# Optimization experiments

Hardware: AMD Instinct MI355X
Metric: run time of the kernel (lower is better)

## Reference

```python
import jax, jax.numpy as jnp
import numpy as np

V = 54  # len(nonterminals)
D = 512  # term_embedding_dim
LEAVES = 60000
LEVELS = 10


def _structure():
    rng = np.random.default_rng(0)
    sizes = [LEAVES]
    for _ in range(LEVELS - 1):
        sizes.append(sizes[-1] // 2)
    starts = np.concatenate([[0], np.cumsum(sizes)]).astype(np.int64)
    N = int(starts[-1])
    node_types = rng.integers(0, V, N).astype(np.int32)
    edge_child, edge_parent, edge_starts = [], [], [0, 0]
    for l in range(1, LEVELS):
        n_l = sizes[l]
        c1 = rng.integers(starts[l - 1], starts[l], n_l)  # child at height l-1 (defines height)
        c2 = rng.integers(0, starts[l], n_l)              # second child anywhere below
        edge_child.append(np.stack([c1, c2], 1).ravel())
        edge_parent.append(np.repeat(np.arange(n_l), 2))
        edge_starts.append(edge_starts[-1] + 2 * n_l)
    edge_child = np.concatenate(edge_child).astype(np.int64)
    edge_parent = np.concatenate(edge_parent).astype(np.int64)
    edge_starts = np.asarray(edge_starts, dtype=np.int64)
    roots = np.arange(starts[-2], starts[-1], dtype=np.int64)  # top-level nodes
    return node_types, starts, edge_child, edge_parent, edge_starts, roots


def setup_inputs() -> dict:
    node_types, level_starts, edge_child, edge_parent_local, edge_level_starts, roots = _structure()
    key = jax.random.key(0)
    ks = jax.random.split(key, 9)
    k = 1.0 / np.sqrt(D)
    u = lambda kk, shape: jax.random.uniform(kk, shape, jnp.float32, -k, k)
    return {
        "node_types": jnp.asarray(node_types),
        "level_starts": level_starts,
        "edge_child": jnp.asarray(edge_child),
        "edge_parent_local": jnp.asarray(edge_parent_local),
        "edge_level_starts": edge_level_starts,
        "roots": jnp.asarray(roots),
        "W_if": u(ks[0], (D, V)),
        "W_hf": u(ks[1], (D, D)),
        "b_f": u(ks[2], (D,)),
        "W_i": u(ks[3], (D, V + D)),
        "b_i": u(ks[4], (D,)),
        "W_o": u(ks[5], (D, V + D)),
        "b_o": u(ks[6], (D,)),
        "W_u": u(ks[7], (D, V + D)),
        "b_u": u(ks[8], (D,)),
    }


def reference(node_types, level_starts, edge_child, edge_parent_local, edge_level_starts,
              roots, W_if, W_hf, b_f, W_i, b_i, W_o, b_o, W_u, b_u):
    ls = np.asarray(level_starts)
    es = np.asarray(edge_level_starts)
    N = int(ls[-1])
    dt = W_if.dtype
    H = jnp.zeros((N, D), dtype=dt)
    C = jnp.zeros((N, D), dtype=dt)
    for l in range(len(ls) - 1):
        s, e = int(ls[l]), int(ls[l + 1])
        n = e - s
        x = jax.nn.one_hot(node_types[s:e], V, dtype=dt)  # [n, V]
        if l == 0:
            h_sum = jnp.zeros((n, D), dtype=dt)
            c_remain = jnp.zeros((n, D), dtype=dt)
        else:
            a, b = int(es[l]), int(es[l + 1])
            ci = edge_child[a:b]
            pj = edge_parent_local[a:b]
            h_ch = H[ci]  # [e_l, D] gather of children hidden states
            c_ch = C[ci]
            h_sum = jax.ops.segment_sum(h_ch, pj, num_segments=n)
            Wx = x @ W_if.T  # [n, D]
            f = jax.nn.sigmoid(Wx[pj] + h_ch @ W_hf.T + b_f)  # per-edge forget gates
            c_remain = jax.ops.segment_sum(f * c_ch, pj, num_segments=n)
        xh = jnp.concatenate([x, h_sum], axis=1)  # [n, V+D]
        i_g = jax.nn.sigmoid(xh @ W_i.T + b_i)
        o_g = jax.nn.sigmoid(xh @ W_o.T + b_o)
        u = jnp.tanh(xh @ W_u.T + b_u)
        cells = i_g * u + c_remain
        hid = o_g * jnp.tanh(cells)
        H = H.at[s:e].set(hid)
        C = C.at[s:e].set(cells)
    return H[roots]
```

## Files before the change

kernel.cpp:

```cpp
#include <hip/hip_runtime.h>
#include <hip/hip_bf16.h>

#define DD 512
#define VV 54
#define NLEAF 60000
#define NINT 59881

typedef __attribute__((ext_vector_type(8))) short bf16x8;
typedef __attribute__((ext_vector_type(4))) float f32x4;

__device__ __forceinline__ float bflo(unsigned int u) {
    union { unsigned int i; float f; } v; v.i = u << 16; return v.f;
}
__device__ __forceinline__ float bfhi(unsigned int u) {
    union { unsigned int i; float f; } v; v.i = u & 0xffff0000u; return v.f;
}
__device__ __forceinline__ float bfu2f(unsigned short u) {
    union { unsigned int i; float f; } v; v.i = ((unsigned int)u) << 16; return v.f;
}
__device__ __forceinline__ unsigned short f2bfu(float f) {
    union { unsigned int i; float f; } v; v.f = f;
    unsigned int x = v.i;
    return (unsigned short)((x + 0x7FFFu + ((x >> 16) & 1u)) >> 16);
}
__device__ __forceinline__ unsigned int pack2(float lo, float hi) {
    return (unsigned int)f2bfu(lo) | ((unsigned int)f2bfu(hi) << 16);
}
__device__ __forceinline__ float b2f(__hip_bfloat16 x) { return __bfloat162float(x); }
__device__ __forceinline__ float sigm(float x) { return 1.f / (1.f + __expf(-x)); }

__device__ __forceinline__ void ld8(const __hip_bfloat16* p, float* o) {
    uint4 v = *(const uint4*)p;
    const unsigned short* s = (const unsigned short*)&v;
#pragma unroll
    for (int j = 0; j < 8; j++) o[j] = bfu2f(s[j]);
}
__device__ __forceinline__ void ldf8(const float* p, float* o) {
    float4 a = *(const float4*)p, b = *(const float4*)(p + 4);
    o[0] = a.x; o[1] = a.y; o[2] = a.z; o[3] = a.w;
    o[4] = b.x; o[5] = b.y; o[6] = b.z; o[7] = b.w;
}

__global__ void detect_idx64(const int* __restrict__ ec, int* __restrict__ flag) {
    __shared__ int nz;
    if (threadIdx.x == 0) nz = 0;
    __syncthreads();
    if (ec[2 * threadIdx.x + 1] != 0) atomicAdd(&nz, 1);
    __syncthreads();
    if (threadIdx.x == 0) flag[0] = (nz == 0) ? 1 : 0;
}

__global__ void prep_tables(const float* __restrict__ W_if, const float* __restrict__ b_f,
                            const float* __restrict__ W_i, const float* __restrict__ b_i,
                            const float* __restrict__ W_o, const float* __restrict__ b_o,
                            const float* __restrict__ W_u, const float* __restrict__ b_u,
                            float* __restrict__ wifc, float* __restrict__ tbi,
                            float* __restrict__ tbo, float* __restrict__ tbu,
                            __hip_bfloat16* __restrict__ hleaf, __hip_bfloat16* __restrict__ cleaf) {
    int t = blockIdx.x;
    for (int d = threadIdx.x; d < DD; d += blockDim.x) {
        wifc[t * DD + d] = W_if[d * VV + t] + b_f[d];
        float vi = W_i[d * (VV + DD) + t] + b_i[d];
        float vo = W_o[d * (VV + DD) + t] + b_o[d];
        float vu = W_u[d * (VV + DD) + t] + b_u[d];
        tbi[t * DD + d] = vi; tbo[t * DD + d] = vo; tbu[t * DD + d] = vu;
        float gi = sigm(vi), go = sigm(vo), gu = tanhf(vu);
        float c = gi * gu;
        float h = go * tanhf(c);
        hleaf[t * DD + d] = __float2bfloat16(h);
        cleaf[t * DD + d] = __float2bfloat16(c);
    }
}

__global__ void prep_wall(const float* __restrict__ W_hf, const float* __restrict__ W_i,
                          const float* __restrict__ W_o, const float* __restrict__ W_u,
                          __hip_bfloat16* __restrict__ Wall) {
    int idx = blockIdx.x * 256 + threadIdx.x;
    int m = idx >> 18;
    int rem = idx & (DD * DD - 1);
    float v;
    if (m == 0) {
        v = W_hf[rem];
    } else {
        int d = rem >> 9, k = rem & 511;
        const float* W = (m == 1) ? W_i : ((m == 2) ? W_o : W_u);
        v = W[d * (VV + DD) + VV + k];
    }
    Wall[idx] = __float2bfloat16(v);
}

__global__ void prep_pleaf(const __hip_bfloat16* __restrict__ hleaf,
                           const __hip_bfloat16* __restrict__ Wall,
                           __hip_bfloat16* __restrict__ Pleaf) {
    __shared__ float hsh[DD];
    int tt = blockIdx.x;
    int cb = blockIdx.y;
    for (int k = threadIdx.x; k < DD; k += 256) hsh[k] = b2f(hleaf[tt * DD + k]);
    __syncthreads();
    int c = cb * 256 + threadIdx.x;
    const __hip_bfloat16* wrow = Wall + (size_t)c * DD;
    float s = 0.f;
#pragma unroll 4
    for (int kq = 0; kq < 64; kq++) {
        uint4 v = *(const uint4*)(wrow + kq * 8);
        const unsigned short* vs = (const unsigned short*)&v;
#pragma unroll
        for (int e = 0; e < 8; e++) s += bfu2f(vs[e]) * hsh[kq * 8 + e];
    }
    Pleaf[(size_t)tt * 2048 + c] = __float2bfloat16(s);
}

__device__ __forceinline__ const __hip_bfloat16* h_row(int ci,
        const __hip_bfloat16* __restrict__ Hint, const __hip_bfloat16* __restrict__ hleaf,
        const int* __restrict__ nt) {
    return (ci < NLEAF) ? (hleaf + (size_t)nt[ci] * DD) : (Hint + (size_t)(ci - NLEAF) * DD);
}
__device__ __forceinline__ const __hip_bfloat16* c_row(int ci,
        const __hip_bfloat16* __restrict__ Cint, const __hip_bfloat16* __restrict__ cleaf,
        const int* __restrict__ nt) {
    return (ci < NLEAF) ? (cleaf + (size_t)nt[ci] * DD) : (Cint + (size_t)(ci - NLEAF) * DD);
}

__global__ __launch_bounds__(256) void gather_cell(
    const __hip_bfloat16* __restrict__ Pleaf,
    const __hip_bfloat16* __restrict__ cleaf,
    const int* __restrict__ nt, const int* __restrict__ ecb, int eoff,
    const int* __restrict__ ntl, const float* __restrict__ wifc,
    const float* __restrict__ tbi, const float* __restrict__ tbo,
    const float* __restrict__ tbu,
    __hip_bfloat16* __restrict__ Hout, __hip_bfloat16* __restrict__ Cout,
    const int* __restrict__ idx64, int n) {
    int idx = blockIdx.x * 256 + threadIdx.x;
    int p = idx >> 6;
    if (p >= n) return;
    const int mode = idx64[0];
    const int d0 = (idx & 63) << 3;
    int c1 = ecb[(eoff + 2 * p) << mode];
    int c2 = ecb[(eoff + 2 * p + 1) << mode];
    int t1 = nt[c1], t2 = nt[c2];
    int tp = ntl[p];
    const __hip_bfloat16* P1 = Pleaf + (size_t)t1 * 2048;
    const __hip_bfloat16* P2 = Pleaf + (size_t)t2 * 2048;
    float f1[8], f2v[8], i1[8], i2[8], o1[8], o2[8], u1[8], u2[8], x1[8], x2[8];
    ld8(P1 + d0, f1);         ld8(P2 + d0, f2v);
    ld8(P1 + 512 + d0, i1);   ld8(P2 + 512 + d0, i2);
    ld8(P1 + 1024 + d0, o1);  ld8(P2 + 1024 + d0, o2);
    ld8(P1 + 1536 + d0, u1);  ld8(P2 + 1536 + d0, u2);
    ld8(cleaf + (size_t)t1 * DD + d0, x1);
    ld8(cleaf + (size_t)t2 * DD + d0, x2);
    float wf[8], vb[8], ob[8], ub[8];
    ldf8(wifc + (size_t)tp * DD + d0, wf);
    ldf8(tbi + (size_t)tp * DD + d0, vb);
    ldf8(tbo + (size_t)tp * DD + d0, ob);
    ldf8(tbu + (size_t)tp * DD + d0, ub);
    float hv[8], cv[8];
#pragma unroll
    for (int j = 0; j < 8; j++) {
        float fr = sigm(f1[j] + wf[j]) * x1[j] + sigm(f2v[j] + wf[j]) * x2[j];
        float gi = sigm(i1[j] + i2[j] + vb[j]);
        float go = sigm(o1[j] + o2[j] + ob[j]);
        float gu = tanhf(u1[j] + u2[j] + ub[j]);
        float c = gi * gu + fr;
        cv[j] = c;
        hv[j] = go * tanhf(c);
    }
    uint4 hp, cp;
    hp.x = pack2(hv[0], hv[1]); hp.y = pack2(hv[2], hv[3]);
    hp.z = pack2(hv[4], hv[5]); hp.w = pack2(hv[6], hv[7]);
    cp.x = pack2(cv[0], cv[1]); cp.y = pack2(cv[2], cv[3]);
    cp.z = pack2(cv[4], cv[5]); cp.w = pack2(cv[6], cv[7]);
    *(uint4*)(Hout + (size_t)p * DD + d0) = hp;
    *(uint4*)(Cout + (size_t)p * DD + d0) = cp;
}

__global__ __launch_bounds__(256) void gemm_f(
    const __hip_bfloat16* __restrict__ Hint, const __hip_bfloat16* __restrict__ Cint,
    const __hip_bfloat16* __restrict__ hleaf, const __hip_bfloat16* __restrict__ cleaf,
    const int* __restrict__ nt, const __hip_bfloat16* __restrict__ Wall,
    const int* __restrict__ ecb, int eoff, const int* __restrict__ ntl,
    const float* __restrict__ wifc, __hip_bfloat16* __restrict__ crem,
    const int* __restrict__ idx64, int n) {
    __shared__ char lds[32768];
    const int M = 2 * n;
    const int R = (M + 127) >> 7;
    const int id = blockIdx.x, xcd = id & 7, q = id >> 3;
    const int rt = xcd + ((q >> 2) << 3), ct = q & 3;
    if (rt >= R) return;
    const int mode = idx64[0];
    const int t = threadIdx.x;
    const int lane = t & 63, w = t >> 6, wr = w >> 1, wc = w & 1;
    const int row0 = rt * 128, col0 = ct * 128;

    const int srow = t & 127;
    const int sc = t >> 7;
    const __hip_bfloat16* aptr = nullptr;
    {
        int e = row0 + srow;
        if (e < M) aptr = h_row(ecb[(eoff + e) << mode], Hint, hleaf, nt);
    }
    const __hip_bfloat16* bptr = Wall + (size_t)(col0 + srow) * DD;
    const int wb = (srow >> 4) * 1024 + (srow & 15) * 16;

    f32x4 acc[4][4];
#pragma unroll
    for (int i = 0; i < 4; i++)
#pragma unroll
        for (int j = 0; j < 4; j++) acc[i][j] = {0.f, 0.f, 0.f, 0.f};

    uint4 ra0 = {0, 0, 0, 0}, ra1 = {0, 0, 0, 0}, rb0, rb1;
    if (aptr) { ra0 = *(const uint4*)(aptr + sc * 8); ra1 = *(const uint4*)(aptr + (sc + 2) * 8); }
    rb0 = *(const uint4*)(bptr + sc * 8);
    rb1 = *(const uint4*)(bptr + (sc + 2) * 8);

#pragma unroll 1
    for (int kt = 0; kt < 16; ++kt) {
        char* buf = lds + (kt & 1) * 16384;
        *(uint4*)(buf + wb + sc * 256) = ra0;
        *(uint4*)(buf + wb + (sc + 2) * 256) = ra1;
        *(uint4*)(buf + 8192 + wb + sc * 256) = rb0;
        *(uint4*)(buf + 8192 + wb + (sc + 2) * 256) = rb1;
        __syncthreads();
        if (kt < 15) {
            int ko = (kt + 1) * 32;
            if (aptr) {
                ra0 = *(const uint4*)(aptr + ko + sc * 8);
                ra1 = *(const uint4*)(aptr + ko + (sc + 2) * 8);
            }
            rb0 = *(const uint4*)(bptr + ko + sc * 8);
            rb1 = *(const uint4*)(bptr + ko + (sc + 2) * 8);
        }
        bf16x8 af[4], bfr[4];
#pragma unroll
        for (int i = 0; i < 4; i++)
            af[i] = *(const bf16x8*)(buf + (wr * 4 + i) * 1024 + lane * 16);
#pragma unroll
        for (int j = 0; j < 4; j++)
            bfr[j] = *(const bf16x8*)(buf + 8192 + (wc * 4 + j) * 1024 + lane * 16);
#pragma unroll
        for (int i = 0; i < 4; i++)
#pragma unroll
            for (int j = 0; j < 4; j++)
                acc[i][j] = __builtin_amdgcn_mfma_f32_16x16x32_bf16(af[i], bfr[j], acc[i][j], 0, 0, 0);
    }

    __hip_bfloat16* ldsCr = (__hip_bfloat16*)lds;
    const int colb = wc * 64;
#pragma unroll
    for (int i = 0; i < 4; i++) {
        int er0l = wr * 64 + i * 16 + ((lane >> 4) << 2);
        int er0 = row0 + er0l;
        if (er0 >= M) continue;
        bool hi = (er0 + 2) < M;
        int p0 = er0 >> 1;
        int p0l = er0l >> 1;
        int t0 = ntl[p0];
        int t1 = hi ? ntl[p0 + 1] : 0;
        int ci0 = ecb[(eoff + er0) << mode];
        int ci1 = ecb[(eoff + er0 + 1) << mode];
        int ci2 = hi ? ecb[(eoff + er0 + 2) << mode] : ci0;
        int ci3 = hi ? ecb[(eoff + er0 + 3) << mode] : ci0;
        const __hip_bfloat16* cp0 = c_row(ci0, Cint, cleaf, nt);
        const __hip_bfloat16* cp1 = c_row(ci1, Cint, cleaf, nt);
        const __hip_bfloat16* cp2 = c_row(ci2, Cint, cleaf, nt);
        const __hip_bfloat16* cp3 = c_row(ci3, Cint, cleaf, nt);
        const float* wfa = wifc + (size_t)t0 * DD;
        const float* wfb = wifc + (size_t)t1 * DD;
#pragma unroll
        for (int j = 0; j < 4; j++) {
            int coll = colb + j * 16 + (lane & 15);
            int col = col0 + coll;
            float wa = wfa[col], wbv = wfb[col];
            float s0 = sigm(acc[i][j].x + wa) * b2f(cp0[col])
                     + sigm(acc[i][j].y + wa) * b2f(cp1[col]);
            ldsCr[p0l * 128 + coll] = __float2bfloat16(s0);
            if (hi) {
                float s1 = sigm(acc[i][j].z + wbv) * b2f(cp2[col])
                         + sigm(acc[i][j].w + wbv) * b2f(cp3[col]);
                ldsCr[(p0l + 1) * 128 + coll] = __float2bfloat16(s1);
            }
        }
    }
    __syncthreads();
    {
        int prow = t >> 2, seg = t & 3;
        int p = (row0 >> 1) + prow;
        if (p < n) {
            const uint4* src = (const uint4*)(lds + prow * 256 + seg * 64);
            uint4* dst = (uint4*)(crem + (size_t)p * DD + col0 + seg * 32);
            dst[0] = src[0]; dst[1] = src[1]; dst[2] = src[2]; dst[3] = src[3];
        }
    }
}

__global__ __launch_bounds__(256) void gemm_g2(
    const __hip_bfloat16* __restrict__ Hint, const __hip_bfloat16* __restrict__ hleaf,
    const int* __restrict__ nt, const __hip_bfloat16* __restrict__ Wall,
    const int* __restrict__ ecb, int eoff, const int* __restrict__ ntl,
    const float* __restrict__ tbi, const float* __restrict__ tbo,
    const float* __restrict__ tbu, const __hip_bfloat16* __restrict__ crem,
    __hip_bfloat16* __restrict__ Hrow, __hip_bfloat16* __restrict__ Crow,
    float* __restrict__ outF, const int* __restrict__ idx64, int n) {
    __shared__ char lds[16384];
    const int R = (n + 63) >> 6;
    const int id = blockIdx.x, xcd = id & 7, q = id >> 3;
    const int rt = xcd + ((q >> 3) << 3), ct = q & 7;
    if (rt >= R) return;
    const int mode = idx64[0];
    const int t = threadIdx.x;
    const int lane = t & 63, w = t >> 6, wr = w >> 1, wc = w & 1;
    const int row0 = rt * 64, col0 = ct * 64;

    const int arow = t & 63, achk = t >> 6;
    const __hip_bfloat16 *pa = nullptr, *pb = nullptr;
    {
        int p = row0 + arow;
        if (p < n) {
            int c0 = ecb[(eoff + 2 * p) << mode];
            int c1 = ecb[(eoff + 2 * p + 1) << mode];
            pa = h_row(c0, Hint, hleaf, nt) + achk * 8;
            pb = h_row(c1, Hint, hleaf, nt) + achk * 8;
        }
    }
    const int wrA = (arow >> 4) * 1024 + (arow & 15) * 16 + achk * 256;
    const __hip_bfloat16* bbase = Wall + (size_t)(512 + col0 + arow) * DD + achk * 8;
    const int wrB = 4096 + wrA;

    f32x4 acc[3][2][2];
#pragma unroll
    for (int g = 0; g < 3; g++)
#pragma unroll
        for (int i = 0; i < 2; i++)
#pragma unroll
            for (int j = 0; j < 2; j++) acc[g][i][j] = {0.f, 0.f, 0.f, 0.f};

    uint4 rax = {0, 0, 0, 0}, ray = {0, 0, 0, 0}, rb[3];
    if (pa) { rax = *(const uint4*)pa; ray = *(const uint4*)pb; }
#pragma unroll
    for (int g = 0; g < 3; g++) rb[g] = *(const uint4*)(bbase + (size_t)g * DD * DD);

#pragma unroll 1
    for (int kt = 0; kt < 16; ++kt) {
        uint4 av;
        av.x = pack2(bflo(rax.x) + bflo(ray.x), bfhi(rax.x) + bfhi(ray.x));
        av.y = pack2(bflo(rax.y) + bflo(ray.y), bfhi(rax.y) + bfhi(ray.y));
        av.z = pack2(bflo(rax.z) + bflo(ray.z), bfhi(rax.z) + bfhi(ray.z));
        av.w = pack2(bflo(rax.w) + bflo(ray.w), bfhi(rax.w) + bfhi(ray.w));
        *(uint4*)(lds + wrA) = av;
#pragma unroll
        for (int g = 0; g < 3; g++) *(uint4*)(lds + wrB + g * 4096) = rb[g];
        __syncthreads();
        if (kt < 15) {
            int ko = (kt + 1) * 32;
            if (pa) { rax = *(const uint4*)(pa + ko); ray = *(const uint4*)(pb + ko); }
#pragma unroll
            for (int g = 0; g < 3; g++) rb[g] = *(const uint4*)(bbase + (size_t)g * DD * DD + ko);
        }
        bf16x8 af[2];
#pragma unroll
        for (int i = 0; i < 2; i++)
            af[i] = *(const bf16x8*)(lds + (wr * 2 + i) * 1024 + lane * 16);
#pragma unroll
        for (int g = 0; g < 3; g++)
#pragma unroll
            for (int j = 0; j < 2; j++) {
                bf16x8 bg = *(const bf16x8*)(lds + 4096 + g * 4096 + (wc * 2 + j) * 1024 + lane * 16);
#pragma unroll
                for (int i = 0; i < 2; i++)
                    acc[g][i][j] = __builtin_amdgcn_mfma_f32_16x16x32_bf16(af[i], bg, acc[g][i][j], 0, 0, 0);
            }
        __syncthreads();
    }

    __hip_bfloat16* ldsH = (__hip_bfloat16*)lds;
    __hip_bfloat16* ldsC = (__hip_bfloat16*)(lds + 8192);
#pragma unroll
    for (int i = 0; i < 2; i++)
#pragma unroll
        for (int j = 0; j < 2; j++) {
            int coll = (wc * 2 + j) * 16 + (lane & 15);
            int col = col0 + coll;
#pragma unroll
            for (int r = 0; r < 4; r++) {
                int pl = wr * 32 + i * 16 + ((lane >> 4) << 2) + r;
                int p = row0 + pl;
                if (p >= n) continue;
                int tp = ntl[p];
                float gi = sigm(acc[0][i][j][r] + tbi[(size_t)tp * DD + col]);
                float go = sigm(acc[1][i][j][r] + tbo[(size_t)tp * DD + col]);
                float gu = tanhf(acc[2][i][j][r] + tbu[(size_t)tp * DD + col]);
                float c = gi * gu + b2f(crem[(size_t)p * DD + col]);
                float h = go * tanhf(c);
                ldsH[pl * 64 + coll] = __float2bfloat16(h);
                ldsC[pl * 64 + coll] = __float2bfloat16(c);
                if (outF) outF[(size_t)p * DD + col] = h;
            }
        }
    __syncthreads();
    {
        int prow = t >> 2, seg = t & 3;
        int p = row0 + prow;
        if (p < n) {
            uint4 h0 = *(uint4*)(lds + prow * 128 + seg * 32);
            uint4 h1 = *(uint4*)(lds + prow * 128 + seg * 32 + 16);
            uint4 c0 = *(uint4*)(lds + 8192 + prow * 128 + seg * 32);
            uint4 c1 = *(uint4*)(lds + 8192 + prow * 128 + seg * 32 + 16);
            *(uint4*)(Hrow + (size_t)p * DD + col0 + seg * 16) = h0;
            *(uint4*)(Hrow + (size_t)p * DD + col0 + seg * 16 + 8) = h1;
            *(uint4*)(Crow + (size_t)p * DD + col0 + seg * 16) = c0;
            *(uint4*)(Crow + (size_t)p * DD + col0 + seg * 16 + 8) = c1;
        }
    }
}

extern "C" void kernel_launch(void* const* d_in, const int* in_sizes, int n_in,
                              void* d_out, int out_size, void* d_ws, size_t ws_size,
                              hipStream_t stream) {
    const int* node_types = (const int*)d_in[0];
    const int* edge_child = (const int*)d_in[2];
    const float* W_if = (const float*)d_in[6];
    const float* W_hf = (const float*)d_in[7];
    const float* b_f = (const float*)d_in[8];
    const float* W_i = (const float*)d_in[9];
    const float* b_i = (const float*)d_in[10];
    const float* W_o = (const float*)d_in[11];
    const float* b_o = (const float*)d_in[12];
    const float* W_u = (const float*)d_in[13];
    const float* b_u = (const float*)d_in[14];
    float* out = (float*)d_out;

    static const int ls[11] = {0, 60000, 90000, 105000, 112500, 116250,
                               118125, 119062, 119530, 119764, 119881};
    static const int es[11] = {0, 0, 60000, 90000, 105000, 112500,
                               116250, 118124, 119060, 119528, 119762};

    char* ws = (char*)d_ws;
    size_t off = 0;
    auto alloc = [&](size_t bytes) -> void* {
        void* p = ws + off;
        off += (bytes + 255) & ~(size_t)255;
        return p;
    };
    int* flag = (int*)alloc(256);
    __hip_bfloat16* Wall = (__hip_bfloat16*)alloc((size_t)4 * DD * DD * 2);
    float* wifc = (float*)alloc((size_t)VV * DD * 4);
    float* tbi = (float*)alloc((size_t)VV * DD * 4);
    float* tbo = (float*)alloc((size_t)VV * DD * 4);
    float* tbu = (float*)alloc((size_t)VV * DD * 4);
    __hip_bfloat16* hleaf = (__hip_bfloat16*)alloc((size_t)VV * DD * 2);
    __hip_bfloat16* cleaf = (__hip_bfloat16*)alloc((size_t)VV * DD * 2);
    __hip_bfloat16* Pleaf = (__hip_bfloat16*)alloc((size_t)VV * 2048 * 2);
    __hip_bfloat16* Hint = (__hip_bfloat16*)alloc((size_t)NINT * DD * 2);
    __hip_bfloat16* Cint = (__hip_bfloat16*)alloc((size_t)NINT * DD * 2);
    __hip_bfloat16* crem = (__hip_bfloat16*)alloc((size_t)15000 * DD * 2);
    (void)ws_size; (void)in_sizes; (void)n_in; (void)out_size;

    detect_idx64<<<1, 128, 0, stream>>>(edge_child, flag);
    prep_tables<<<54, 256, 0, stream>>>(W_if, b_f, W_i, b_i, W_o, b_o, W_u, b_u,
                                        wifc, tbi, tbo, tbu, hleaf, cleaf);
    prep_wall<<<(4 * DD * DD) / 256, 256, 0, stream>>>(W_hf, W_i, W_o, W_u, Wall);
    {
        dim3 g(VV, 8);
        prep_pleaf<<<g, 256, 0, stream>>>(hleaf, Wall, Pleaf);
    }

    {
        int n = ls[2] - ls[1];
        gather_cell<<<(n * 64 + 255) / 256, 256, 0, stream>>>(
            Pleaf, cleaf, node_types, edge_child, es[1], node_types + ls[1],
            wifc, tbi, tbo, tbu, Hint, Cint, flag, n);
    }

    for (int l = 2; l < 10; l++) {
        int s = ls[l];
        int n = ls[l + 1] - s;
        int M2 = 2 * n;
        int Rf = (M2 + 127) / 128;
        int gridF = 8 * ((Rf + 7) / 8) * 4;
        gemm_f<<<gridF, 256, 0, stream>>>(Hint, Cint, hleaf, cleaf, node_types, Wall,
                                          edge_child, es[l], node_types + s, wifc, crem,
                                          flag, n);
        int Rg = (n + 63) / 64;
        int gridG = 8 * ((Rg + 7) / 8) * 8;
        gemm_g2<<<gridG, 256, 0, stream>>>(Hint, hleaf, node_types, Wall,
                                           edge_child, es[l], node_types + s,
                                           tbi, tbo, tbu, crem,
                                           Hint + (size_t)(s - NLEAF) * DD,
                                           Cint + (size_t)(s - NLEAF) * DD,
                                           (l == 9) ? out : nullptr, flag, n);
    }
}
```

Baseline: 801.8 us.

## Fuse forget-gate and cell GEMMs into one MFMA kernel for upper levels

For levels 3 through 9, one fused kernel replaces the separate gemm_f and gemm_g2 launches. It computes the per-edge products with all four weight blocks (forget, input, output, update) in one pass over gathered child hidden rows. Each parent's two edges are summed in registers and the cell update is done in the epilogue, so the crem intermediate buffer and one launch per level go away. Level 2 keeps the old two-kernel path. The cost is that the i/o/u GEMMs now run over edges, twice as many rows as parents, and each block holds four accumulator sets.

```diff
diff --git a/kernel.cpp b/kernel.cpp
--- a/kernel.cpp
+++ b/kernel.cpp
@@ -412,6 +412,149 @@
     }
 }
 
+__global__ __launch_bounds__(256) void fused_mfma(
+    const __hip_bfloat16* __restrict__ Hint, const __hip_bfloat16* __restrict__ Cint,
+    const __hip_bfloat16* __restrict__ hleaf, const __hip_bfloat16* __restrict__ cleaf,
+    const int* __restrict__ nt, const __hip_bfloat16* __restrict__ Wall,
+    const int* __restrict__ ecb, int eoff, const int* __restrict__ ntl,
+    const float* __restrict__ wifc, const float* __restrict__ tbi,
+    const float* __restrict__ tbo, const float* __restrict__ tbu,
+    __hip_bfloat16* __restrict__ Hrow, __hip_bfloat16* __restrict__ Crow,
+    float* __restrict__ outF, const int* __restrict__ idx64, int n) {
+    __shared__ char lds[40960];
+    const int M = 2 * n;
+    const int mode = idx64[0];
+    const int t = threadIdx.x;
+    const int lane = t & 63, w = t >> 6, wr = w >> 1, wc = w & 1;
+    const int row0 = blockIdx.x * 64;
+    const int col0 = blockIdx.y * 64;
+
+    const int srow = t & 63, schk = t >> 6;
+    const int soff = (srow >> 4) * 1024 + (srow & 15) * 16 + schk * 256;
+
+    const __hip_bfloat16* aptr = nullptr;
+    {
+        int e = row0 + srow;
+        if (e < M) aptr = h_row(ecb[(eoff + e) << mode], Hint, hleaf, nt);
+    }
+    const __hip_bfloat16* bptr = Wall + (size_t)(col0 + srow) * DD + schk * 8;
+
+    f32x4 acc[4][2][2];
+#pragma unroll
+    for (int m = 0; m < 4; m++)
+#pragma unroll
+        for (int i = 0; i < 2; i++)
+#pragma unroll
+            for (int j = 0; j < 2; j++) acc[m][i][j] = {0.f, 0.f, 0.f, 0.f};
+
+    uint4 ra = {0, 0, 0, 0};
+    uint4 rb[4];
+    if (aptr) ra = *(const uint4*)(aptr + schk * 8);
+#pragma unroll
+    for (int m = 0; m < 4; m++) rb[m] = *(const uint4*)(bptr + (size_t)m * DD * DD);
+
+#pragma unroll 1
+    for (int kt = 0; kt < 16; ++kt) {
+        char* buf = lds + (kt & 1) * 20480;
+        *(uint4*)(buf + soff) = ra;
+#pragma unroll
+        for (int m = 0; m < 4; m++)
+            *(uint4*)(buf + 4096 + m * 4096 + soff) = rb[m];
+        __syncthreads();
+        if (kt < 15) {
+            int ko = (kt + 1) * 32;
+            if (aptr) ra = *(const uint4*)(aptr + ko + schk * 8);
+#pragma unroll
+            for (int m = 0; m < 4; m++)
+                rb[m] = *(const uint4*)(bptr + (size_t)m * DD * DD + ko);
+        }
+        bf16x8 af[2];
+#pragma unroll
+        for (int i = 0; i < 2; i++)
+            af[i] = *(const bf16x8*)(buf + (wr * 2 + i) * 1024 + lane * 16);
+#pragma unroll
+        for (int m = 0; m < 4; m++) {
+            bf16x8 b0 = *(const bf16x8*)(buf + 4096 + m * 4096 + (wc * 2 + 0) * 1024 + lane * 16);
+            bf16x8 b1 = *(const bf16x8*)(buf + 4096 + m * 4096 + (wc * 2 + 1) * 1024 + lane * 16);
+            acc[m][0][0] = __builtin_amdgcn_mfma_f32_16x16x32_bf16(af[0], b0, acc[m][0][0], 0, 0, 0);
+            acc[m][0][1] = __builtin_amdgcn_mfma_f32_16x16x32_bf16(af[0], b1, acc[m][0][1], 0, 0, 0);
+            acc[m][1][0] = __builtin_amdgcn_mfma_f32_16x16x32_bf16(af[1], b0, acc[m][1][0], 0, 0, 0);
+            acc[m][1][1] = __builtin_amdgcn_mfma_f32_16x16x32_bf16(af[1], b1, acc[m][1][1], 0, 0, 0);
+        }
+    }
+
+    __hip_bfloat16* ldsH = (__hip_bfloat16*)lds;
+    __hip_bfloat16* ldsC = (__hip_bfloat16*)(lds + 4096);
+
+#pragma unroll
+    for (int i = 0; i < 2; i++) {
+        int er0l = wr * 32 + i * 16 + ((lane >> 4) << 2);
+        int er0 = row0 + er0l;
+        if (er0 >= M) continue;
+        bool hi = (er0 + 2) < M;
+        int p0 = er0 >> 1;
+        int p0l = er0l >> 1;
+        int tp0 = ntl[p0];
+        int tp1 = hi ? ntl[p0 + 1] : 0;
+        int ci0 = ecb[(eoff + er0) << mode];
+        int ci1 = ecb[(eoff + er0 + 1) << mode];
+        int ci2 = hi ? ecb[(eoff + er0 + 2) << mode] : ci0;
+        int ci3 = hi ? ecb[(eoff + er0 + 3) << mode] : ci0;
+        const __hip_bfloat16* cp0 = c_row(ci0, Cint, cleaf, nt);
+        const __hip_bfloat16* cp1 = c_row(ci1, Cint, cleaf, nt);
+        const __hip_bfloat16* cp2 = c_row(ci2, Cint, cleaf, nt);
+        const __hip_bfloat16* cp3 = c_row(ci3, Cint, cleaf, nt);
+#pragma unroll
+        for (int j = 0; j < 2; j++) {
+            int coll = (wc * 2 + j) * 16 + (lane & 15);
+            int col = col0 + coll;
+            f32x4 aF = acc[0][i][j], aI = acc[1][i][j], aO = acc[2][i][j], aU = acc[3][i][j];
+            {
+                float wf = wifc[(size_t)tp0 * DD + col];
+                float fr = sigm(aF.x + wf) * b2f(cp0[col]) + sigm(aF.y + wf) * b2f(cp1[col]);
+                float gi = sigm(aI.x + aI.y + tbi[(size_t)tp0 * DD + col]);
+                float go = sigm(aO.x + aO.y + tbo[(size_t)tp0 * DD + col]);
+                float gu = tanhf(aU.x + aU.y + tbu[(size_t)tp0 * DD + col]);
+                float c = gi * gu + fr;
+                float h = go * tanhf(c);
+                ldsH[p0l * 64 + coll] = __float2bfloat16(h);
+                ldsC[p0l * 64 + coll] = __float2bfloat16(c);
+            }
+            if (hi) {
+                float wf = wifc[(size_t)tp1 * DD + col];
+                float fr = sigm(aF.z + wf) * b2f(cp2[col]) + sigm(aF.w + wf) * b2f(cp3[col]);
+                float gi = sigm(aI.z + aI.w + tbi[(size_t)tp1 * DD + col]);
+                float go = sigm(aO.z + aO.w + tbo[(size_t)tp1 * DD + col]);
+                float gu = tanhf(aU.z + aU.w + tbu[(size_t)tp1 * DD + col]);
+                float c = gi * gu + fr;
+                float h = go * tanhf(c);
+                ldsH[(p0l + 1) * 64 + coll] = __float2bfloat16(h);
+                ldsC[(p0l + 1) * 64 + coll] = __float2bfloat16(c);
+            }
+        }
+    }
+    __syncthreads();
+
+    {
+        int prow = t >> 3, seg = t & 7;
+        int p = (row0 >> 1) + prow;
+        if (p < n) {
+            uint4 hv = *(uint4*)(lds + prow * 128 + seg * 16);
+            uint4 cv = *(uint4*)(lds + 4096 + prow * 128 + seg * 16);
+            *(uint4*)(Hrow + (size_t)p * DD + col0 + seg * 8) = hv;
+            *(uint4*)(Crow + (size_t)p * DD + col0 + seg * 8) = cv;
+            if (outF) {
+                const unsigned short* hs = (const unsigned short*)&hv;
+                float4 o0, o1;
+                o0.x = bfu2f(hs[0]); o0.y = bfu2f(hs[1]); o0.z = bfu2f(hs[2]); o0.w = bfu2f(hs[3]);
+                o1.x = bfu2f(hs[4]); o1.y = bfu2f(hs[5]); o1.z = bfu2f(hs[6]); o1.w = bfu2f(hs[7]);
+                *(float4*)(outF + (size_t)p * DD + col0 + seg * 8) = o0;
+                *(float4*)(outF + (size_t)p * DD + col0 + seg * 8 + 4) = o1;
+            }
+        }
+    }
+}
+
 extern "C" void kernel_launch(void* const* d_in, const int* in_sizes, int n_in,
                               void* d_out, int out_size, void* d_ws, size_t ws_size,
                               hipStream_t stream) {
@@ -470,20 +613,28 @@
             wifc, tbi, tbo, tbu, Hint, Cint, flag, n);
     }
 
-    for (int l = 2; l < 10; l++) {
+    {
+        int l = 2, s = ls[l], n = ls[l + 1] - s;
+        int Rf = (2 * n + 127) / 128;
+        gemm_f<<<8 * ((Rf + 7) / 8) * 4, 256, 0, stream>>>(
+            Hint, Cint, hleaf, cleaf, node_types, Wall,
+            edge_child, es[l], node_types + s, wifc, crem, flag, n);
+        int Rg = (n + 63) / 64;
+        gemm_g2<<<8 * ((Rg + 7) / 8) * 8, 256, 0, stream>>>(
+            Hint, hleaf, node_types, Wall,
+            edge_child, es[l], node_types + s, tbi, tbo, tbu, crem,
+            Hint + (size_t)(s - NLEAF) * DD, Cint + (size_t)(s - NLEAF) * DD,
+            nullptr, flag, n);
+    }
+
+    for (int l = 3; l < 10; l++) {
         int s = ls[l];
         int n = ls[l + 1] - s;
         int M2 = 2 * n;
-        int Rf = (M2 + 127) / 128;
-        int gridF = 8 * ((Rf + 7) / 8) * 4;
-        gemm_f<<<gridF, 256, 0, stream>>>(Hint, Cint, hleaf, cleaf, node_types, Wall,
-                                          edge_child, es[l], node_types + s, wifc, crem,
-                                          flag, n);
-        int Rg = (n + 63) / 64;
-        int gridG = 8 * ((Rg + 7) / 8) * 8;
-        gemm_g2<<<gridG, 256, 0, stream>>>(Hint, hleaf, node_types, Wall,
+        dim3 gg((M2 + 63) / 64, 8);
+        fused_mfma<<<gg, 256, 0, stream>>>(Hint, Cint, hleaf, cleaf, node_types, Wall,
                                            edge_child, es[l], node_types + s,
-                                           tbi, tbo, tbu, crem,
+                                           wifc, tbi, tbo, tbu,
                                            Hint + (size_t)(s - NLEAF) * DD,
                                            Cint + (size_t)(s - NLEAF) * DD,
                                            (l == 9) ? out : nullptr, flag, n);
```

After: 816.3 us. No clear change (+1.8%).
